# Performance work log

Measured on AMD Instinct MI355X. Metric: run time of the kernel, lower is better.

Reference implementation:

```python
import jax, jax.numpy as jnp
import numpy as np

N_SAMPLES = 524288
N_FEATURES = 64
N_GATES = 64
N_OUTPUTS = 8
BASE = N_FEATURES + 2                # X cols + constant-0 col + constant-1 col
MAX_CONN = BASE + N_GATES            # 130
TEMPERATURE = 1.0                    # forward() default
NEG = -1e9                           # mask value for not-yet-available slots


def setup_inputs() -> dict:
    key = jax.random.key(0)
    k1, k2, k3 = jax.random.split(key, 3)
    X = jax.random.uniform(k1, (N_SAMPLES, N_FEATURES), dtype=jnp.float32)
    gate_weights = jax.random.normal(k2, (N_GATES, MAX_CONN), dtype=jnp.float32) * 0.1
    output_weights = jax.random.normal(k3, (N_GATES, N_OUTPUTS), dtype=jnp.float32) * 0.1
    output_scale = jnp.ones((N_OUTPUTS,), dtype=jnp.float32)
    return {"X": X, "gate_weights": gate_weights,
            "output_weights": output_weights, "output_scale": output_scale}


def reference(X, gate_weights, output_weights, output_scale):
    n = X.shape[0]
    # available = [X | zeros | ones | gate slots]; gate slots filled sequentially
    buf = jnp.concatenate([
        X,
        jnp.zeros((n, 1), X.dtype),
        jnp.ones((n, 1), X.dtype),
        jnp.zeros((n, N_GATES), X.dtype),
    ], axis=1)                                            # [N, MAX_CONN]

    # Connection selection is data-independent: softmax over the first
    # (BASE + gate_idx) slots of each gate's weight row, then top-2.
    col_ids = jnp.arange(MAX_CONN)
    avail_mask = col_ids[None, :] < (BASE + jnp.arange(N_GATES))[:, None]
    logits = jnp.where(avail_mask, gate_weights / TEMPERATURE, NEG)
    probs = jax.nn.softmax(logits, axis=1)                # [n_gates, MAX_CONN]
    _, top2 = jax.lax.top_k(probs, 2)                     # [n_gates, 2]

    # Sequential NAND chain over a small fixed number of gates (structural loop).
    gate_outs = []
    for i in range(N_GATES):
        a = buf[:, top2[i, 0]]                            # [N]
        b = buf[:, top2[i, 1]]
        g = 1.0 - a * b                                   # continuous NAND
        gate_outs.append(g)
        buf = buf.at[:, BASE + i].set(g)

    gate_matrix = jnp.stack(gate_outs, axis=1)            # [N, n_gates]
    outputs = (gate_matrix @ output_weights) * output_scale
    return outputs
```

## Files before the change

### kernel.cpp

```cpp
#include <hip/hip_runtime.h>
#include <hip/hip_fp16.h>

#define N_SAMPLES 524288
#define N_FEATURES 64
#define N_GATES 64
#define N_OUTPUTS 8
#define BASE_COLS 66
#define MAX_CONN 130

#define CH 8
#define MAXSLOTS 512
#define GWS_STR 131
#define FB_STR 65

typedef float v2f __attribute__((ext_vector_type(2)));

__device__ __forceinline__ void top2_ins(float x, int j, float& v1, int& i1, float& v2, int& i2) {
    bool gt1 = (x > v1) || (x == v1 && j < i1);
    bool gt2 = (x > v2) || (x == v2 && j < i2);
    if (gt1) { v2 = v1; i2 = i1; v1 = x; i1 = j; }
    else if (gt2) { v2 = x; i2 = j; }
}

__global__ __launch_bounds__(256) void plan_kernel(
    const float* __restrict__ gw,
    int* __restrict__ slots,
    int* __restrict__ nch)
{
    __shared__ float gws[N_GATES * GWS_STR];
    __shared__ float pv1[4][N_GATES], pv2[4][N_GATES];
    __shared__ int   pi1[4][N_GATES], pi2[4][N_GATES];
    __shared__ int   rec[MAXSLOTS];

    const int tid = threadIdx.x;

    const float4* gw4 = (const float4*)gw;
    for (int k = tid; k < (N_GATES * MAX_CONN) / 4; k += 256) {
        float4 v = gw4[k];
        int base = 4 * k;
        #pragma unroll
        for (int e = 0; e < 4; ++e) {
            int idx = base + e;
            int gi  = idx / MAX_CONN;
            int jj  = idx - gi * MAX_CONN;
            gws[gi * GWS_STR + jj] = (&v.x)[e];
        }
    }
    __syncthreads();

    {
        const int g = tid & 63, s = tid >> 6;
        const int avail = BASE_COLS + g;
        int j0 = s * 33;
        int j1 = j0 + 33; if (j1 > avail) j1 = avail;
        float v1 = -1e30f, v2 = -1e30f;
        int   i1 = 0x7fffffff, i2 = 0x7fffffff;
        const float* w = gws + g * GWS_STR;
        for (int j = j0; j < j1; ++j)
            top2_ins(w[j], j, v1, i1, v2, i2);
        pv1[s][g] = v1; pi1[s][g] = i1;
        pv2[s][g] = v2; pi2[s][g] = i2;
    }
    __syncthreads();

    if (tid >= 64) return;
    const int l = tid;

    float v1 = -1e30f, v2 = -1e30f;
    int   i1 = 0x7fffffff, i2 = 0x7fffffff;
    #pragma unroll
    for (int s = 0; s < 4; ++s) {
        top2_ins(pv1[s][l], pi1[s][l], v1, i1, v2, i2);
        top2_ins(pv2[s][l], pi2[s][l], v1, i1, v2, i2);
    }

    const bool ga = (i1 >= BASE_COLS), gb = (i2 >= BASE_COLS);
    const int  pa = ga ? (i1 - BASE_COLS) : 0;
    const int  pb = gb ? (i2 - BASE_COLS) : 0;
    int lvl = 0;
    bool changed = true;
    while (__any(changed)) {
        int la = __shfl(lvl, pa);
        int lb = __shfl(lvl, pb);
        int nl = lvl;
        if (ga && la + 1 > nl) nl = la + 1;
        if (gb && lb + 1 > nl) nl = lb + 1;
        changed = (nl != lvl);
        lvl = nl;
    }

    int myslot = 0, running = 0, assigned = 0;
    for (int L = 0; assigned < N_GATES; ++L) {
        unsigned long long mask = __ballot(lvl == L);
        int c = __popcll(mask);
        if (c) {
            if (lvl == L) {
                int pos = __popcll(mask & ((1ull << l) - 1ull));
                myslot = running + pos;
            }
            running += (c + CH - 1) & ~(CH - 1);
            assigned += c;
        }
    }
    const int ns = running;

    const int pad = 64 | (64 << 8) | (64 << 16);
    for (int q = l; q < ns; q += 64) rec[q] = pad;
    rec[myslot] = i1 | (i2 << 8) | (l << 16);
    for (int q = l; q < ns; q += 64) slots[q] = rec[q];
    if (l == 0) *nch = ns / CH;
}

__global__ __launch_bounds__(64) void circuit_kernel(
    const float* __restrict__ X,
    const int*   __restrict__ slots,
    const int*   __restrict__ nch,
    const float* __restrict__ ow,
    const float* __restrict__ scale,
    float*       __restrict__ out)
{
    __shared__ __half2 fbuf[N_FEATURES * FB_STR];
    __shared__ __half2 gbuf[(N_GATES + 1) * 64];

    const int t = threadIdx.x;
    const long long s0 = (long long)blockIdx.x * 128;

    const float4* Xv = (const float4*)(X + s0 * N_FEATURES);
    #pragma unroll
    for (int k = 0; k < 16; ++k) {
        int q  = k * 64 + t;
        int c4 = q & 15;
        int j  = q >> 4;
        float4 va = Xv[(2 * j)     * 16 + c4];
        float4 vb = Xv[(2 * j + 1) * 16 + c4];
        int c = 4 * c4;
        fbuf[(c + 0) * FB_STR + j] = __halves2half2(__float2half(va.x), __float2half(vb.x));
        fbuf[(c + 1) * FB_STR + j] = __halves2half2(__float2half(va.y), __float2half(vb.y));
        fbuf[(c + 2) * FB_STR + j] = __halves2half2(__float2half(va.z), __float2half(vb.z));
        fbuf[(c + 3) * FB_STR + j] = __halves2half2(__float2half(va.w), __float2half(vb.w));
    }
    __syncthreads();

    const int nchunks = __builtin_amdgcn_readfirstlane(*nch);
    const __half2 one2  = __half2half2(__float2half(1.0f));
    const __half2 zero2 = __half2half2(__float2half(0.0f));

    const int4* sl4 = (const int4*)slots;
    for (int ch = 0; ch < nchunks; ++ch) {
        int4 wa = sl4[ch * 2];
        int4 wb = sl4[ch * 2 + 1];
        int sl[CH] = {wa.x, wa.y, wa.z, wa.w, wb.x, wb.y, wb.z, wb.w};

        __half2 av[CH], bv[CH];
        int wr[CH];
        #pragma unroll
        for (int k = 0; k < CH; ++k) {
            int sv = __builtin_amdgcn_readfirstlane(sl[k]);
            int ea =  sv        & 255;
            int eb = (sv >> 8)  & 255;
            wr[k]  = (sv >> 16) & 255;
            av[k] = (ea >= BASE_COLS) ? gbuf[(ea - BASE_COLS) * 64 + t]
                  : (ea == 64)        ? zero2
                  : (ea == 65)        ? one2
                                      : fbuf[ea * FB_STR + t];
            bv[k] = (eb >= BASE_COLS) ? gbuf[(eb - BASE_COLS) * 64 + t]
                  : (eb == 64)        ? zero2
                  : (eb == 65)        ? one2
                                      : fbuf[eb * FB_STR + t];
        }
        #pragma unroll
        for (int k = 0; k < CH; ++k) {
            __half2 gv = __hfma2(__hneg2(av[k]), bv[k], one2);
            gbuf[wr[k] * 64 + t] = gv;
        }
    }

    v2f acc[N_OUTPUTS];
    #pragma unroll
    for (int o = 0; o < N_OUTPUTS; ++o) { acc[o].x = 0.0f; acc[o].y = 0.0f; }

    #pragma unroll 4
    for (int g = 0; g < N_GATES; ++g) {
        __half2 gv = gbuf[g * 64 + t];
        v2f g2; g2.x = __low2float(gv); g2.y = __high2float(gv);
        #pragma unroll
        for (int o = 0; o < N_OUTPUTS; ++o) {
            float w = ow[g * N_OUTPUTS + o];
            v2f wv; wv.x = w; wv.y = w;
            acc[o] = __builtin_elementwise_fma(g2, wv, acc[o]);
        }
    }

    float sc[N_OUTPUTS];
    #pragma unroll
    for (int o = 0; o < N_OUTPUTS; ++o) sc[o] = scale[o];

    float4* outv = (float4*)(out + (s0 + 2 * t) * N_OUTPUTS);
    outv[0] = make_float4(acc[0].x * sc[0], acc[1].x * sc[1], acc[2].x * sc[2], acc[3].x * sc[3]);
    outv[1] = make_float4(acc[4].x * sc[4], acc[5].x * sc[5], acc[6].x * sc[6], acc[7].x * sc[7]);
    outv[2] = make_float4(acc[0].y * sc[0], acc[1].y * sc[1], acc[2].y * sc[2], acc[3].y * sc[3]);
    outv[3] = make_float4(acc[4].y * sc[4], acc[5].y * sc[5], acc[6].y * sc[6], acc[7].y * sc[7]);
}

extern "C" void kernel_launch(void* const* d_in, const int* in_sizes, int n_in,
                              void* d_out, int out_size, void* d_ws, size_t ws_size,
                              hipStream_t stream)
{
    const float* X     = (const float*)d_in[0];
    const float* gw    = (const float*)d_in[1];
    const float* ow    = (const float*)d_in[2];
    const float* scale = (const float*)d_in[3];
    float* out = (float*)d_out;

    char* ws  = (char*)d_ws;
    int* slots = (int*)ws;
    int* nch   = (int*)(ws + 2048);

    plan_kernel<<<1, 256, 0, stream>>>(gw, slots, nch);

    const int blocks = N_SAMPLES / 128;
    circuit_kernel<<<blocks, 64, 0, stream>>>(X, slots, nch, ow, scale, out);
}
```

Measured before the change: 271.0 us.

## Split gate levels across four waves with barrier-separated per-wave gate streams

The plan kernel now emits four per-wave instruction streams, where the gates of each dependency level are dealt round-robin across waves and separated by barrier markers. The circuit kernel runs 256-thread blocks in which each wave evaluates its share of gates and folds each gate into the output accumulators as it goes. The partial sums are then reduced across waves through shared memory. The layout also changes: features, the constant rows and the gates share one XOR-swizzled half2 buffer, which removes the branchy source selection and padding bank conflicts. In exchange, each level costs a block-wide barrier, and the output weights are reloaded per gate inside the loop.

```diff
diff --git a/kernel.cpp b/kernel.cpp
--- a/kernel.cpp
+++ b/kernel.cpp
@@ -8,10 +8,11 @@
 #define BASE_COLS 66
 #define MAX_CONN 130
 
-#define CH 8
-#define MAXSLOTS 512
+#define NWAVES 4
+#define MAXW 192
+#define ROWS 131
 #define GWS_STR 131
-#define FB_STR 65
+#define PAD_SLOT (64 | (64 << 8) | (130 << 16))
 
 typedef float v2f __attribute__((ext_vector_type(2)));
 
@@ -24,13 +25,12 @@
 
 __global__ __launch_bounds__(256) void plan_kernel(
     const float* __restrict__ gw,
-    int* __restrict__ slots,
-    int* __restrict__ nch)
+    int* __restrict__ stream)
 {
     __shared__ float gws[N_GATES * GWS_STR];
     __shared__ float pv1[4][N_GATES], pv2[4][N_GATES];
     __shared__ int   pi1[4][N_GATES], pi2[4][N_GATES];
-    __shared__ int   rec[MAXSLOTS];
+    __shared__ int   streamL[NWAVES * MAXW];
 
     const int tid = threadIdx.x;
 
@@ -89,122 +89,137 @@
         lvl = nl;
     }
 
-    int myslot = 0, running = 0, assigned = 0;
-    for (int L = 0; assigned < N_GATES; ++L) {
+    for (int q = l; q < NWAVES * MAXW; q += 64) streamL[q] = -2;
+
+    int p_base = 0, assigned = 0;
+    int myW = 0, myP = 0;
+    for (int L = 0; L < 64 && assigned < 64; ++L) {
         unsigned long long mask = __ballot(lvl == L);
         int c = __popcll(mask);
-        if (c) {
-            if (lvl == L) {
-                int pos = __popcll(mask & ((1ull << l) - 1ull));
-                myslot = running + pos;
-            }
-            running += (c + CH - 1) & ~(CH - 1);
-            assigned += c;
-        }
-    }
-    const int ns = running;
-
-    const int pad = 64 | (64 << 8) | (64 << 16);
-    for (int q = l; q < ns; q += 64) rec[q] = pad;
-    rec[myslot] = i1 | (i2 << 8) | (l << 16);
-    for (int q = l; q < ns; q += 64) slots[q] = rec[q];
-    if (l == 0) *nch = ns / CH;
-}
-
-__global__ __launch_bounds__(64) void circuit_kernel(
+        if (!c) continue;
+        int m = (c + NWAVES - 1) >> 2;
+        if (lvl == L) {
+            int r = __popcll(mask & ((1ull << l) - 1ull));
+            myW = r & 3; myP = p_base + (r >> 2);
+        }
+        if (l <= m) {
+            int val = (l == m) ? -1 : PAD_SLOT;
+            #pragma unroll
+            for (int wv = 0; wv < NWAVES; ++wv)
+                streamL[wv * MAXW + p_base + l] = val;
+        }
+        p_base += m + 1;
+        assigned += c;
+    }
+
+    streamL[myW * MAXW + myP] = i1 | (i2 << 8) | ((BASE_COLS + l) << 16) | (l << 24);
+
+    for (int q = l; q < NWAVES * MAXW; q += 64) stream[q] = streamL[q];
+}
+
+__global__ __launch_bounds__(256, 4) void circuit_kernel(
     const float* __restrict__ X,
-    const int*   __restrict__ slots,
-    const int*   __restrict__ nch,
+    const int*   __restrict__ stream,
     const float* __restrict__ ow,
     const float* __restrict__ scale,
     float*       __restrict__ out)
 {
-    __shared__ __half2 fbuf[N_FEATURES * FB_STR];
-    __shared__ __half2 gbuf[(N_GATES + 1) * 64];
-
-    const int t = threadIdx.x;
+    __shared__ __half2 buf[ROWS * 64];
+
+    const int tid = threadIdx.x;
+    const int w = tid >> 6, t = tid & 63;
     const long long s0 = (long long)blockIdx.x * 128;
 
+    const int* st = stream + w * MAXW;
+    const int sv0 = st[t], sv1 = st[64 + t], sv2 = st[128 + t];
+
     const float4* Xv = (const float4*)(X + s0 * N_FEATURES);
     #pragma unroll
-    for (int k = 0; k < 16; ++k) {
-        int q  = k * 64 + t;
+    for (int k = 0; k < 4; ++k) {
+        int q  = k * 256 + tid;
         int c4 = q & 15;
         int j  = q >> 4;
         float4 va = Xv[(2 * j)     * 16 + c4];
         float4 vb = Xv[(2 * j + 1) * 16 + c4];
         int c = 4 * c4;
-        fbuf[(c + 0) * FB_STR + j] = __halves2half2(__float2half(va.x), __float2half(vb.x));
-        fbuf[(c + 1) * FB_STR + j] = __halves2half2(__float2half(va.y), __float2half(vb.y));
-        fbuf[(c + 2) * FB_STR + j] = __halves2half2(__float2half(va.z), __float2half(vb.z));
-        fbuf[(c + 3) * FB_STR + j] = __halves2half2(__float2half(va.w), __float2half(vb.w));
-    }
-    __syncthreads();
-
-    const int nchunks = __builtin_amdgcn_readfirstlane(*nch);
-    const __half2 one2  = __half2half2(__float2half(1.0f));
-    const __half2 zero2 = __half2half2(__float2half(0.0f));
-
-    const int4* sl4 = (const int4*)slots;
-    for (int ch = 0; ch < nchunks; ++ch) {
-        int4 wa = sl4[ch * 2];
-        int4 wb = sl4[ch * 2 + 1];
-        int sl[CH] = {wa.x, wa.y, wa.z, wa.w, wb.x, wb.y, wb.z, wb.w};
-
-        __half2 av[CH], bv[CH];
-        int wr[CH];
+        buf[(c + 0) * 64 + (j ^ ((c + 0) & 31))] = __halves2half2(__float2half(va.x), __float2half(vb.x));
+        buf[(c + 1) * 64 + (j ^ ((c + 1) & 31))] = __halves2half2(__float2half(va.y), __float2half(vb.y));
+        buf[(c + 2) * 64 + (j ^ ((c + 2) & 31))] = __halves2half2(__float2half(va.z), __float2half(vb.z));
+        buf[(c + 3) * 64 + (j ^ ((c + 3) & 31))] = __halves2half2(__float2half(va.w), __float2half(vb.w));
+    }
+    if (tid < 64)        buf[64 * 64 + tid]              = __half2half2(__float2half(0.0f));
+    else if (tid < 128)  buf[65 * 64 + ((tid - 64) ^ 1)] = __half2half2(__float2half(1.0f));
+    __syncthreads();
+
+    const __half2 one2 = __half2half2(__float2half(1.0f));
+    v2f acc[N_OUTPUTS];
+    #pragma unroll
+    for (int o = 0; o < N_OUTPUTS; ++o) { acc[o].x = 0.0f; acc[o].y = 0.0f; }
+
+    int p = 0;
+    while (true) {
+        int sv = (p < 64)  ? __builtin_amdgcn_readlane(sv0, p)
+               : (p < 128) ? __builtin_amdgcn_readlane(sv1, p - 64)
+                           : __builtin_amdgcn_readlane(sv2, p - 128);
+        ++p;
+        if (sv < 0) {
+            if (sv == -1) { __syncthreads(); continue; }
+            break;
+        }
+        const int ra  =  sv        & 255;
+        const int rb  = (sv >> 8)  & 255;
+        const int wrr = (sv >> 16) & 255;
+        const int gid = (sv >> 24) & 127;
+        __half2 a = buf[ra * 64 + (t ^ (ra & 31))];
+        __half2 b = buf[rb * 64 + (t ^ (rb & 31))];
+        __half2 gv = __hfma2(__hneg2(a), b, one2);
+        buf[wrr * 64 + (t ^ (wrr & 31))] = gv;
+        if (wrr != 130) {
+            v2f g2; g2.x = __low2float(gv); g2.y = __high2float(gv);
+            #pragma unroll
+            for (int o = 0; o < N_OUTPUTS; ++o) {
+                float wt = ow[gid * N_OUTPUTS + o];
+                v2f wv; wv.x = wt; wv.y = wt;
+                acc[o] = __builtin_elementwise_fma(g2, wv, acc[o]);
+            }
+        }
+    }
+
+    __syncthreads();
+    float2* red = (float2*)buf;
+    #pragma unroll
+    for (int o = 0; o < N_OUTPUTS; ++o) {
+        float2 v; v.x = acc[o].x; v.y = acc[o].y;
+        red[(w * N_OUTPUTS + o) * 64 + t] = v;
+    }
+    __syncthreads();
+
+    if (w == 0) {
+        float sc[N_OUTPUTS];
         #pragma unroll
-        for (int k = 0; k < CH; ++k) {
-            int sv = __builtin_amdgcn_readfirstlane(sl[k]);
-            int ea =  sv        & 255;
-            int eb = (sv >> 8)  & 255;
-            wr[k]  = (sv >> 16) & 255;
-            av[k] = (ea >= BASE_COLS) ? gbuf[(ea - BASE_COLS) * 64 + t]
-                  : (ea == 64)        ? zero2
-                  : (ea == 65)        ? one2
-                                      : fbuf[ea * FB_STR + t];
-            bv[k] = (eb >= BASE_COLS) ? gbuf[(eb - BASE_COLS) * 64 + t]
-                  : (eb == 64)        ? zero2
-                  : (eb == 65)        ? one2
-                                      : fbuf[eb * FB_STR + t];
-        }
-        #pragma unroll
-        for (int k = 0; k < CH; ++k) {
-            __half2 gv = __hfma2(__hneg2(av[k]), bv[k], one2);
-            gbuf[wr[k] * 64 + t] = gv;
-        }
-    }
-
-    v2f acc[N_OUTPUTS];
-    #pragma unroll
-    for (int o = 0; o < N_OUTPUTS; ++o) { acc[o].x = 0.0f; acc[o].y = 0.0f; }
-
-    #pragma unroll 4
-    for (int g = 0; g < N_GATES; ++g) {
-        __half2 gv = gbuf[g * 64 + t];
-        v2f g2; g2.x = __low2float(gv); g2.y = __high2float(gv);
+        for (int o = 0; o < N_OUTPUTS; ++o) sc[o] = scale[o];
+
+        v2f s[N_OUTPUTS];
         #pragma unroll
         for (int o = 0; o < N_OUTPUTS; ++o) {
-            float w = ow[g * N_OUTPUTS + o];
-            v2f wv; wv.x = w; wv.y = w;
-            acc[o] = __builtin_elementwise_fma(g2, wv, acc[o]);
-        }
-    }
-
-    float sc[N_OUTPUTS];
-    #pragma unroll
-    for (int o = 0; o < N_OUTPUTS; ++o) sc[o] = scale[o];
-
-    float4* outv = (float4*)(out + (s0 + 2 * t) * N_OUTPUTS);
-    outv[0] = make_float4(acc[0].x * sc[0], acc[1].x * sc[1], acc[2].x * sc[2], acc[3].x * sc[3]);
-    outv[1] = make_float4(acc[4].x * sc[4], acc[5].x * sc[5], acc[6].x * sc[6], acc[7].x * sc[7]);
-    outv[2] = make_float4(acc[0].y * sc[0], acc[1].y * sc[1], acc[2].y * sc[2], acc[3].y * sc[3]);
-    outv[3] = make_float4(acc[4].y * sc[4], acc[5].y * sc[5], acc[6].y * sc[6], acc[7].y * sc[7]);
+            float2 r0 = red[(0 * N_OUTPUTS + o) * 64 + t];
+            float2 r1 = red[(1 * N_OUTPUTS + o) * 64 + t];
+            float2 r2 = red[(2 * N_OUTPUTS + o) * 64 + t];
+            float2 r3 = red[(3 * N_OUTPUTS + o) * 64 + t];
+            s[o].x = ((r0.x + r1.x) + (r2.x + r3.x)) * sc[o];
+            s[o].y = ((r0.y + r1.y) + (r2.y + r3.y)) * sc[o];
+        }
+        float4* outv = (float4*)(out + (s0 + 2 * t) * N_OUTPUTS);
+        outv[0] = make_float4(s[0].x, s[1].x, s[2].x, s[3].x);
+        outv[1] = make_float4(s[4].x, s[5].x, s[6].x, s[7].x);
+        outv[2] = make_float4(s[0].y, s[1].y, s[2].y, s[3].y);
+        outv[3] = make_float4(s[4].y, s[5].y, s[6].y, s[7].y);
+    }
 }
 
 extern "C" void kernel_launch(void* const* d_in, const int* in_sizes, int n_in,
                               void* d_out, int out_size, void* d_ws, size_t ws_size,
-                              hipStream_t stream)
+                              hipStream_t stream_)
 {
     const float* X     = (const float*)d_in[0];
     const float* gw    = (const float*)d_in[1];
@@ -212,12 +227,10 @@
     const float* scale = (const float*)d_in[3];
     float* out = (float*)d_out;
 
-    char* ws  = (char*)d_ws;
-    int* slots = (int*)ws;
-    int* nch   = (int*)(ws + 2048);
-
-    plan_kernel<<<1, 256, 0, stream>>>(gw, slots, nch);
+    int* stream_ws = (int*)d_ws;
+
+    plan_kernel<<<1, 256, 0, stream_>>>(gw, stream_ws);
 
     const int blocks = N_SAMPLES / 128;
-    circuit_kernel<<<blocks, 64, 0, stream>>>(X, slots, nch, ow, scale, out);
-}
+    circuit_kernel<<<blocks, 256, 0, stream_>>>(X, stream_ws, ow, scale, out);
+}
```

Result: faster. 233.0 us (-14.0%).

## Unify feature/gate LDS buffer and fuse output projection into gate loop

Applied to the files above, without the earlier changes.

Feature columns, the constant-0 and constant-1 columns, and gate outputs now share one padded LDS buffer. Every connection becomes a single indexed load, with no per-gate select chain to pick between constants, features and gates. The output matmul is folded into the gate evaluation loop: each slot carries its gate id and looks up a zero-padded weight row prepared by the plan kernel, so padded slots add nothing. This removes the separate pass that re-read gate outputs from LDS, at the cost of more per-slot FMAs, scalar loads of the table entries, and dropping the barrier after the X load (safe only because each block is a single wavefront).

```diff
diff --git a/kernel.cpp b/kernel.cpp
--- a/kernel.cpp
+++ b/kernel.cpp
@@ -11,7 +11,8 @@
 #define CH 8
 #define MAXSLOTS 512
 #define GWS_STR 131
-#define FB_STR 65
+#define STR 65
+#define PAD_SLOT (64 | (64 << 8) | (130 << 16) | (64 << 24))
 
 typedef float v2f __attribute__((ext_vector_type(2)));
 
@@ -24,13 +25,15 @@
 
 __global__ __launch_bounds__(256) void plan_kernel(
     const float* __restrict__ gw,
-    int* __restrict__ slots,
-    int* __restrict__ nch)
+    const float* __restrict__ ow,
+    int*   __restrict__ tab,
+    float* __restrict__ wS,
+    int*   __restrict__ nrp)
 {
     __shared__ float gws[N_GATES * GWS_STR];
     __shared__ float pv1[4][N_GATES], pv2[4][N_GATES];
     __shared__ int   pi1[4][N_GATES], pi2[4][N_GATES];
-    __shared__ int   rec[MAXSLOTS];
+    __shared__ int   tabL[MAXSLOTS];
 
     const int tid = threadIdx.x;
 
@@ -89,38 +92,37 @@
         lvl = nl;
     }
 
-    int myslot = 0, running = 0, assigned = 0;
-    for (int L = 0; assigned < N_GATES; ++L) {
+    int base = 0, assigned = 0, myslot = 0;
+    for (int L = 0; L < 64 && assigned < 64; ++L) {
         unsigned long long mask = __ballot(lvl == L);
         int c = __popcll(mask);
-        if (c) {
-            if (lvl == L) {
-                int pos = __popcll(mask & ((1ull << l) - 1ull));
-                myslot = running + pos;
-            }
-            running += (c + CH - 1) & ~(CH - 1);
-            assigned += c;
-        }
-    }
-    const int ns = running;
-
-    const int pad = 64 | (64 << 8) | (64 << 16);
-    for (int q = l; q < ns; q += 64) rec[q] = pad;
-    rec[myslot] = i1 | (i2 << 8) | (l << 16);
-    for (int q = l; q < ns; q += 64) slots[q] = rec[q];
-    if (l == 0) *nch = ns / CH;
+        if (!c) continue;
+        if (lvl == L) {
+            int r = __popcll(mask & ((1ull << l) - 1ull));
+            myslot = base + r;
+        }
+        int cpad = (c + CH - 1) & ~(CH - 1);
+        if (l < cpad - c) tabL[base + c + l] = PAD_SLOT;
+        base += cpad;
+        assigned += c;
+    }
+    tabL[myslot] = i1 | (i2 << 8) | ((BASE_COLS + l) << 16) | (l << 24);
+
+    for (int q = l; q < base; q += 64) tab[q] = tabL[q];
+    for (int q = l; q < 65 * N_OUTPUTS; q += 64)
+        wS[q] = (q < N_GATES * N_OUTPUTS) ? ow[q] : 0.0f;
+    if (l == 0) *nrp = base / CH;
 }
 
 __global__ __launch_bounds__(64) void circuit_kernel(
     const float* __restrict__ X,
-    const int*   __restrict__ slots,
-    const int*   __restrict__ nch,
-    const float* __restrict__ ow,
+    const int*   __restrict__ tab,
+    const float* __restrict__ wS,
+    const int*   __restrict__ nrp,
     const float* __restrict__ scale,
     float*       __restrict__ out)
 {
-    __shared__ __half2 fbuf[N_FEATURES * FB_STR];
-    __shared__ __half2 gbuf[(N_GATES + 1) * 64];
+    __shared__ __half2 buf[131 * STR];
 
     const int t = threadIdx.x;
     const long long s0 = (long long)blockIdx.x * 128;
@@ -133,61 +135,54 @@
         int j  = q >> 4;
         float4 va = Xv[(2 * j)     * 16 + c4];
         float4 vb = Xv[(2 * j + 1) * 16 + c4];
-        int c = 4 * c4;
-        fbuf[(c + 0) * FB_STR + j] = __halves2half2(__float2half(va.x), __float2half(vb.x));
-        fbuf[(c + 1) * FB_STR + j] = __halves2half2(__float2half(va.y), __float2half(vb.y));
-        fbuf[(c + 2) * FB_STR + j] = __halves2half2(__float2half(va.z), __float2half(vb.z));
-        fbuf[(c + 3) * FB_STR + j] = __halves2half2(__float2half(va.w), __float2half(vb.w));
-    }
-    __syncthreads();
-
-    const int nchunks = __builtin_amdgcn_readfirstlane(*nch);
-    const __half2 one2  = __half2half2(__float2half(1.0f));
-    const __half2 zero2 = __half2half2(__float2half(0.0f));
-
-    const int4* sl4 = (const int4*)slots;
-    for (int ch = 0; ch < nchunks; ++ch) {
-        int4 wa = sl4[ch * 2];
-        int4 wb = sl4[ch * 2 + 1];
-        int sl[CH] = {wa.x, wa.y, wa.z, wa.w, wb.x, wb.y, wb.z, wb.w};
-
-        __half2 av[CH], bv[CH];
-        int wr[CH];
+        #pragma unroll
+        for (int i = 0; i < 4; ++i)
+            buf[(4 * c4 + i) * STR + j] =
+                __halves2half2(__float2half((&va.x)[i]), __float2half((&vb.x)[i]));
+    }
+    buf[64 * STR + t] = __half2half2(__float2half(0.0f));
+    buf[65 * STR + t] = __half2half2(__float2half(1.0f));
+
+    const int nr = __builtin_amdgcn_readfirstlane(*nrp);
+    const __half2 one2 = __half2half2(__float2half(1.0f));
+
+    v2f acc[N_OUTPUTS];
+    #pragma unroll
+    for (int o = 0; o < N_OUTPUTS; ++o) { acc[o].x = 0.0f; acc[o].y = 0.0f; }
+
+    for (int r = 0; r < nr; ++r) {
+        int sv[CH];
+        #pragma unroll
+        for (int k = 0; k < CH; ++k)
+            sv[k] = __builtin_amdgcn_readfirstlane(tab[r * CH + k]);
+
+        __half2 A[CH], B[CH];
         #pragma unroll
         for (int k = 0; k < CH; ++k) {
-            int sv = __builtin_amdgcn_readfirstlane(sl[k]);
-            int ea =  sv        & 255;
-            int eb = (sv >> 8)  & 255;
-            wr[k]  = (sv >> 16) & 255;
-            av[k] = (ea >= BASE_COLS) ? gbuf[(ea - BASE_COLS) * 64 + t]
-                  : (ea == 64)        ? zero2
-                  : (ea == 65)        ? one2
-                                      : fbuf[ea * FB_STR + t];
-            bv[k] = (eb >= BASE_COLS) ? gbuf[(eb - BASE_COLS) * 64 + t]
-                  : (eb == 64)        ? zero2
-                  : (eb == 65)        ? one2
-                                      : fbuf[eb * FB_STR + t];
-        }
+            int ea = sv[k] & 255;
+            int eb = (sv[k] >> 8) & 255;
+            A[k] = buf[ea * STR + t];
+            B[k] = buf[eb * STR + t];
+        }
+
+        __half2 V[CH];
         #pragma unroll
         for (int k = 0; k < CH; ++k) {
-            __half2 gv = __hfma2(__hneg2(av[k]), bv[k], one2);
-            gbuf[wr[k] * 64 + t] = gv;
-        }
-    }
-
-    v2f acc[N_OUTPUTS];
-    #pragma unroll
-    for (int o = 0; o < N_OUTPUTS; ++o) { acc[o].x = 0.0f; acc[o].y = 0.0f; }
-
-    #pragma unroll 4
-    for (int g = 0; g < N_GATES; ++g) {
-        __half2 gv = gbuf[g * 64 + t];
-        v2f g2; g2.x = __low2float(gv); g2.y = __high2float(gv);
-        #pragma unroll
-        for (int o = 0; o < N_OUTPUTS; ++o) {
-            float w = ow[g * N_OUTPUTS + o];
-            v2f wv; wv.x = w; wv.y = w;
-            acc[o] = __builtin_elementwise_fma(g2, wv, acc[o]);
+            V[k] = __hfma2(__hneg2(A[k]), B[k], one2);
+            int wr = (sv[k] >> 16) & 255;
+            buf[wr * STR + t] = V[k];
+        }
+
+        #pragma unroll
+        for (int k = 0; k < CH; ++k) {
+            int gid = (sv[k] >> 24) & 255;
+            const float* wp = wS + gid * N_OUTPUTS;
+            v2f g2; g2.x = __low2float(V[k]); g2.y = __high2float(V[k]);
+            #pragma unroll
+            for (int o = 0; o < N_OUTPUTS; ++o) {
+                v2f wv; wv.x = wp[o]; wv.y = wp[o];
+                acc[o] = __builtin_elementwise_fma(g2, wv, acc[o]);
+            }
         }
     }
 
@@ -204,7 +199,7 @@
 
 extern "C" void kernel_launch(void* const* d_in, const int* in_sizes, int n_in,
                               void* d_out, int out_size, void* d_ws, size_t ws_size,
-                              hipStream_t stream)
+                              hipStream_t stream_)
 {
     const float* X     = (const float*)d_in[0];
     const float* gw    = (const float*)d_in[1];
@@ -212,12 +207,13 @@
     const float* scale = (const float*)d_in[3];
     float* out = (float*)d_out;
 
-    char* ws  = (char*)d_ws;
-    int* slots = (int*)ws;
-    int* nch   = (int*)(ws + 2048);
-
-    plan_kernel<<<1, 256, 0, stream>>>(gw, slots, nch);
+    char* ws = (char*)d_ws;
+    int*   tab = (int*)ws;
+    float* wS  = (float*)(ws + 2048);
+    int*   nrp = (int*)(ws + 2048 + 2080 + 32);
+
+    plan_kernel<<<1, 256, 0, stream_>>>(gw, ow, tab, wS, nrp);
 
     const int blocks = N_SAMPLES / 128;
-    circuit_kernel<<<blocks, 64, 0, stream>>>(X, slots, nch, ow, scale, out);
-}
+    circuit_kernel<<<blocks, 64, 0, stream_>>>(X, tab, wS, nrp, scale, out);
+}
```

New measurement: 240.6 us. -11.2%, faster.
